# Kernel optimization log

Measured on AMD Instinct MI355X. Metric: run time of the kernel, lower is better.

## Reference

```python
import jax, jax.numpy as jnp
import numpy as np
import math

D_MODEL = 512
EXPAND = 2
D_INNER = EXPAND * D_MODEL          # 1024
HEADDIM = 8
NHEADS = D_INNER // HEADDIM         # 128
NGROUPS = 2
D_STATE = 16
CONV_DIM = D_INNER + 2 * NGROUPS * D_STATE   # 1088
D_IN_PROJ = 2 * D_INNER + 2 * NGROUPS * D_STATE + NHEADS  # 2240
P13 = [(0, 0), (1, 1)]
P31 = [(1, 1), (0, 0)]
P33 = [(1, 1), (1, 1)]


def silu(x):
    return x * jax.nn.sigmoid(x)


def dwconv(x, w, pad):
    # depthwise 2D conv; x: (B,C,H,W), w: (C,1,kh,kw)
    return jax.lax.conv_general_dilated(
        x, w, (1, 1), pad,
        dimension_numbers=('NCHW', 'OIHW', 'NCHW'),
        feature_group_count=x.shape[1])


def interleave_ch(a, b):
    # channel-interleave: out[:, ::2] = a, out[:, 1::2] = b
    Bn, C, Hh, Ww = a.shape
    return jnp.stack([a, b], axis=2).reshape(Bn, 2 * C, Hh, Ww)


def linear_attn(x, dt, A, Bm, Cm, Dp):
    # non-causal linear-attention duality of Mamba2 (grouped heads)
    # x: (B,L,h,p), dt: (B,L,h), A: (h,) negative, Bm/Cm: (B,L,g*ds), Dp: (h,)
    b, L, h, p = x.shape
    g, ds = NGROUPS, D_STATE
    dA = -(dt * A[None, None, :])          # ssd_positive_dA -> positive
    Vs = x * dA[..., None]
    K = Bm.reshape(b, L, g, ds)
    Q = Cm.reshape(b, L, g, ds)
    Vg = Vs.reshape(b, L, h // g, g, p)
    KV = jnp.einsum('blgs,blmgp->bmgsp', K, Vg)       # (b, h/g, g, ds, p)
    y = jnp.einsum('blgs,bmgsp->blmgp', Q, KV)        # (b, L, h/g, g, p)
    y = y + (x * Dp[None, None, :, None]).reshape(b, L, h // g, g, p)
    return y.reshape(b, L, h, p)


def setup_inputs() -> dict:
    key = jax.random.key(0)
    ks = jax.random.split(key, 20)
    Bn, Hh, Ww = 8, 64, 64
    L = Hh * Ww
    u = jax.random.normal(ks[0], (Bn, L, D_MODEL), jnp.float32)
    W_in = jax.random.normal(ks[1], (D_IN_PROJ, D_MODEL), jnp.float32) / math.sqrt(D_MODEL)
    dt = jnp.exp(jax.random.uniform(ks[2], (NHEADS,)) * (math.log(0.1) - math.log(0.001)) + math.log(0.001))
    dt = jnp.clip(dt, 1e-4, None)
    dt_bias = dt + jnp.log(-jnp.expm1(-dt))
    A_log = jnp.log(jax.random.uniform(ks[3], (NHEADS,), minval=1.0, maxval=16.0))
    Dp = jnp.ones((NHEADS,), jnp.float32)

    def cw(k, c, kh, kw):
        return jax.random.normal(k, (c, 1, kh, kw), jnp.float32) / math.sqrt(kh * kw)

    bcC = 2 * NGROUPS * D_STATE // 4  # 16
    w_conv2d = cw(ks[4], CONV_DIM // 2, 3, 3)
    w13x1 = cw(ks[5], D_INNER // 4, 1, 3)
    w31x1 = cw(ks[6], D_INNER // 4, 3, 1)
    w13x2 = cw(ks[7], D_INNER // 4, 1, 3)
    w31x2 = cw(ks[8], D_INNER // 4, 3, 1)
    w13bc1 = cw(ks[9], bcC, 1, 3)
    w31bc1 = cw(ks[10], bcC, 3, 1)
    w13bc2 = cw(ks[11], bcC, 1, 3)
    w31bc2 = cw(ks[12], bcC, 3, 1)
    w_conv2d_z = cw(ks[13], D_INNER, 3, 3)
    ln_g = jnp.ones((D_INNER,), jnp.float32)
    ln_b = jnp.zeros((D_INNER,), jnp.float32)
    scale = jnp.float32(1.0)
    shift = jnp.float32(0.0)
    alpha1 = jnp.float32(1.0)
    alpha2 = jnp.float32(1.0)
    W_out = jax.random.normal(ks[14], (D_MODEL, 2 * D_INNER), jnp.float32) / math.sqrt(2 * D_INNER)
    return dict(u=u, H=Hh, W=Ww, W_in=W_in, dt_bias=dt_bias, A_log=A_log, Dp=Dp,
                w_conv2d=w_conv2d, w13x1=w13x1, w31x1=w31x1, w13x2=w13x2, w31x2=w31x2,
                w13bc1=w13bc1, w31bc1=w31bc1, w13bc2=w13bc2, w31bc2=w31bc2,
                w_conv2d_z=w_conv2d_z, ln_g=ln_g, ln_b=ln_b, scale=scale, shift=shift,
                alpha1=alpha1, alpha2=alpha2, W_out=W_out)


def reference(u, H, W, W_in, dt_bias, A_log, Dp, w_conv2d, w13x1, w31x1, w13x2, w31x2,
              w13bc1, w31bc1, w13bc2, w31bc2, w_conv2d_z, ln_g, ln_b, scale, shift,
              alpha1, alpha2, W_out):
    Bn, L, _ = u.shape
    zxbcdt = u @ W_in.T                                 # (B,L,2240)
    z = zxbcdt[..., :D_INNER]
    xBC = zxbcdt[..., D_INNER:D_INNER + CONV_DIM]
    dt = zxbcdt[..., D_INNER + CONV_DIM:]
    dt = jax.nn.softplus(dt + dt_bias)                  # (B,L,h)

    # even/odd channel-interleave split, reshape to NCHW feature maps
    even = xBC[..., 0::2].reshape(Bn, H, W, -1).transpose(0, 3, 1, 2)
    odd = xBC[..., 1::2].reshape(Bn, H, W, -1).transpose(0, 3, 1, 2)
    even = silu(dwconv(even, w_conv2d, P33))

    oe = odd[:, 0::2]
    oo = odd[:, 1::2]
    x_oe, bc_oe = oe[:, :D_INNER // 4], oe[:, D_INNER // 4:]
    x_oo, bc_oo = oo[:, :D_INNER // 4], oo[:, D_INNER // 4:]
    x_oe = silu(dwconv(dwconv(x_oe, w31x1, P31), w13x1, P13))
    x_oo = silu(dwconv(dwconv(x_oo, w13x2, P13), w31x2, P31))
    bc_oe = silu(dwconv(dwconv(bc_oe, w13bc1, P13), w31bc1, P31))
    bc_oo = silu(dwconv(dwconv(bc_oo, w31bc2, P31), w13bc2, P13))
    xbc_oe = jnp.concatenate([x_oe, bc_oe], axis=1)
    xbc_oo = jnp.concatenate([x_oo, bc_oo], axis=1)
    odd = interleave_ch(xbc_oe, xbc_oo)

    xBCc = interleave_ch(even, odd)                     # (B, CONV_DIM, H, W)
    xBCc = xBCc.transpose(0, 2, 3, 1).reshape(Bn, L, CONV_DIM)
    x = xBCc[..., :D_INNER]
    Bm = xBCc[..., D_INNER:D_INNER + NGROUPS * D_STATE]
    Cm = xBCc[..., D_INNER + NGROUPS * D_STATE:]

    A = -jnp.exp(A_log)
    y = linear_attn(x.reshape(Bn, L, NHEADS, HEADDIM), dt, A, Bm, Cm, Dp)
    y = y.reshape(Bn, L, D_INNER)

    mu = y.mean(-1, keepdims=True)
    var = ((y - mu) ** 2).mean(-1, keepdims=True)
    y = (y - mu) / jnp.sqrt(var + 1e-5) * ln_g + ln_b
    y = y * scale + shift

    zc = z.reshape(Bn, H, W, D_INNER).transpose(0, 3, 1, 2)
    zc = silu(dwconv(zc, w_conv2d_z, P33))
    zc = zc.transpose(0, 2, 3, 1).reshape(Bn, L, D_INNER)

    out = jnp.concatenate([alpha1 * y, alpha2 * zc], axis=-1) @ W_out.T
    return out
```

## Files before the change

kernel.cpp:

```cpp
#include <hip/hip_runtime.h>
#include <hip/hip_bf16.h>
#include <cstdint>
#include <cstddef>

#define HDIM    64
#define WDIM    64
#define LPB     4096
#define DMODEL  512
#define DIN     1024
#define CONVD   1088
#define DPROJ   2240
#define NHEADS  128
#define NCV     2112

using f16    = _Float16;
using f16x4  = __attribute__((ext_vector_type(4))) _Float16;
using f16x8  = __attribute__((ext_vector_type(8))) _Float16;
using f32x4  = __attribute__((ext_vector_type(4))) float;

__device__ __forceinline__ float siluf(float x) { return x / (1.f + __expf(-x)); }

__device__ __forceinline__ void fma_mix_lo(float& acc, unsigned a, unsigned b) {
  asm("v_fma_mix_f32 %0, %1, %2, %0 op_sel_hi:[1,1,0]" : "+v"(acc) : "v"(a), "v"(b));
}
__device__ __forceinline__ void fma_mix_hi(float& acc, unsigned a, unsigned b) {
  asm("v_fma_mix_f32 %0, %1, %2, %0 op_sel:[1,1,0] op_sel_hi:[1,1,0]" : "+v"(acc) : "v"(a), "v"(b));
}
__device__ __forceinline__ void fmixl(float& acc, unsigned a, float b) {
  asm("v_fma_mix_f32 %0, %1, %2, %0 op_sel_hi:[1,0,0]" : "+v"(acc) : "v"(a), "v"(b));
}
__device__ __forceinline__ void fmixh(float& acc, unsigned a, float b) {
  asm("v_fma_mix_f32 %0, %1, %2, %0 op_sel:[1,0,0] op_sel_hi:[1,0,0]" : "+v"(acc) : "v"(a), "v"(b));
}

__global__ __launch_bounds__(256) void k_cvt(const float* __restrict__ in, f16* __restrict__ out) {
  size_t i = ((size_t)blockIdx.x * 256 + threadIdx.x) * 4;
  f32x4 v = *(const f32x4*)(in + i);
  f16x4 o;
  #pragma unroll
  for (int j = 0; j < 4; ++j) o[j] = (f16)v[j];
  *(f16x4*)(out + i) = o;
}

__global__ __launch_bounds__(256) void k_cvt_win(const float* __restrict__ W, f16* __restrict__ out) {
  int i = blockIdx.x * 256 + threadIdx.x;
  int row = i >> 9, col = i & 511;
  float v = (row < DPROJ) ? W[row * 512 + col] : 0.f;
  out[i] = (f16)v;
}

__global__ __launch_bounds__(256) void k_keff(const float* __restrict__ w33,
                       const float* __restrict__ w13x1, const float* __restrict__ w31x1,
                       const float* __restrict__ w13x2, const float* __restrict__ w31x2,
                       const float* __restrict__ w13bc1, const float* __restrict__ w31bc1,
                       const float* __restrict__ w13bc2, const float* __restrict__ w31bc2,
                       const float* __restrict__ wz,
                       f16* __restrict__ keffall) {
  int j = blockIdx.x * 256 + threadIdx.x;
  if (j >= NCV) return;
  if (j < 1024) {
    #pragma unroll
    for (int tap = 0; tap < 9; ++tap) keffall[tap * NCV + j] = (f16)wz[j * 9 + tap];
    return;
  }
  int jj = j - 1024;
  float kh[3] = {0,0,0}, kw[3] = {0,0,0};
  bool dense = ((jj & 1) == 0);
  if (!dense) {
    int m = jj >> 2;
    if ((jj & 3) == 1) {
      if (m < 256) { for (int t=0;t<3;++t){ kh[t]=w31x1[m*3+t];  kw[t]=w13x1[m*3+t];  } }
      else { int q=m-256; for (int t=0;t<3;++t){ kh[t]=w31bc1[q*3+t]; kw[t]=w13bc1[q*3+t]; } }
    } else {
      if (m < 256) { for (int t=0;t<3;++t){ kh[t]=w31x2[m*3+t];  kw[t]=w13x2[m*3+t];  } }
      else { int q=m-256; for (int t=0;t<3;++t){ kh[t]=w31bc2[q*3+t]; kw[t]=w13bc2[q*3+t]; } }
    }
  }
  #pragma unroll
  for (int dh = 0; dh < 3; ++dh)
    #pragma unroll
    for (int dw = 0; dw < 3; ++dw) {
      float v = dense ? w33[(jj >> 1) * 9 + dh*3 + dw] : kh[dh] * kw[dw];
      keffall[(dh*3 + dw) * NCV + j] = (f16)v;
    }
}

template<typename OutT>
__global__ __launch_bounds__(256) void k_gemmf(const f16* __restrict__ A, int lda,
                                               const f16* __restrict__ Bm, int ldb,
                                               OutT* __restrict__ C, int ldc,
                                               int Kseg, int NW, int ntn, int ntmn, long Cseg) {
  __shared__ __align__(16) f16 As[128 * 32];
  __shared__ __align__(16) f16 Bs[128 * 32];

  int nwg = gridDim.x, bid = blockIdx.x;
  int q = nwg >> 3, r = nwg & 7;
  int xcd = bid & 7, loc = bid >> 3;
  int wg  = (xcd < r ? xcd * (q + 1) : r * (q + 1) + (xcd - r) * q) + loc;
  int kseg = wg / ntmn;
  int rem  = wg - kseg * ntmn;
  long m0 = (long)(rem / ntn) * 128;
  long n0 = (long)(rem % ntn) * 128;
  const int kbase = kseg * Kseg;

  const int tid  = threadIdx.x;
  const int w    = tid >> 6, lane = tid & 63;
  const int wr   = w >> 1, wc = w & 1;

  f32x4 acc[4][4];
  #pragma unroll
  for (int i = 0; i < 4; ++i)
    #pragma unroll
    for (int j = 0; j < 4; ++j) acc[i][j] = (f32x4){0.f,0.f,0.f,0.f};

  const int srow = w * 16 + (lane >> 2);
  const int scol = (lane & 3) * 8;
  const long aoff = (m0 + srow) * (long)lda + scol + kbase;
  const long boff = (n0 + srow) * (long)ldb + scol + kbase;
  const int fr = lane & 15;
  const int kc = (lane >> 4) * 8;

  for (int k0 = 0; k0 < Kseg; k0 += 32) {
    #pragma unroll
    for (int i = 0; i < 2; ++i) {
      long ao = aoff + (long)i*64*lda + k0;
      long bo = boff + (long)i*64*ldb + k0;
      int ls = (i*4 + w) * 512;
      __builtin_amdgcn_global_load_lds((const __attribute__((address_space(1))) void*)(A + ao),
                                       (__attribute__((address_space(3))) void*)&As[ls], 16, 0, 0);
      __builtin_amdgcn_global_load_lds((const __attribute__((address_space(1))) void*)(Bm + bo),
                                       (__attribute__((address_space(3))) void*)&Bs[ls], 16, 0, 0);
    }
    __syncthreads();
    f16x8 af[4], bf[4];
    #pragma unroll
    for (int f = 0; f < 4; ++f) {
      af[f] = *(const f16x8*)&As[(wr*64 + f*16 + fr) * 32 + kc];
      bf[f] = *(const f16x8*)&Bs[(wc*64 + f*16 + fr) * 32 + kc];
    }
    #pragma unroll
    for (int i = 0; i < 4; ++i)
      #pragma unroll
      for (int j = 0; j < 4; ++j)
        acc[i][j] = __builtin_amdgcn_mfma_f32_16x16x32_f16(af[i], bf[j], acc[i][j], 0, 0, 0);
    __syncthreads();
  }

  OutT* Cb = C + (long)kseg * Cseg;
  const int cr = (lane >> 4) * 4;
  const int cc = lane & 15;
  #pragma unroll
  for (int i = 0; i < 4; ++i) {
    long rbase = m0 + wr*64 + i*16 + cr;
    #pragma unroll
    for (int j = 0; j < 4; ++j) {
      int col = (int)n0 + wc*64 + j*16 + cc;
      if (col < NW) {
        OutT* cp = Cb + rbase * (long)ldc + col;
        #pragma unroll
        for (int r = 0; r < 4; ++r) cp[(long)r * ldc] = (OutT)acc[i][j][r];
      }
    }
  }
}

__global__ __launch_bounds__(256) void k_red2(const float* __restrict__ part, long seg,
                                              float* __restrict__ out) {
  long i = ((long)blockIdx.x * 256 + threadIdx.x) * 4;
  f32x4 s0 = *(const f32x4*)(part + i);
  f32x4 s1 = *(const f32x4*)(part + seg + i);
  f32x4 o;
  #pragma unroll
  for (int j = 0; j < 4; ++j) o[j] = s0[j] + s1[j];
  *(f32x4*)(out + i) = o;
}

__global__ __launch_bounds__(320) void k_conv_all(const f16* __restrict__ zx,
                                                  const f16* __restrict__ keffall,
                                                  const float* __restrict__ a2_p,
                                                  const float* __restrict__ dt_bias,
                                                  const float* __restrict__ A_log,
                                                  f16* __restrict__ xbc,
                                                  f16* __restrict__ g2,
                                                  float* __restrict__ dAb) {
  int t = threadIdx.x;
  int bid = blockIdx.x, qq = gridDim.x >> 3;
  int l = (bid & 7) * qq + (bid >> 3);
  int h = (l >> 6) & 63, wq = l & 63;
  long rowbase = (long)l * DPROJ;

  if (t < 264) {
    int c = t * 8;
    float acc[8] = {0,0,0,0,0,0,0,0};
    #pragma unroll
    for (int dh = 0; dh < 3; ++dh) {
      int hh = h + dh - 1;
      if (hh < 0 || hh >= HDIM) continue;
      #pragma unroll
      for (int dw = 0; dw < 3; ++dw) {
        int ww = wq + dw - 1;
        if (ww < 0 || ww >= WDIM) continue;
        uint4 v  = *(const uint4*)&zx[rowbase + (long)((dh-1)*WDIM + (dw-1)) * DPROJ + c];
        uint4 wt = *(const uint4*)&keffall[(dh*3 + dw) * NCV + c];
        fma_mix_lo(acc[0], v.x, wt.x);  fma_mix_hi(acc[1], v.x, wt.x);
        fma_mix_lo(acc[2], v.y, wt.y);  fma_mix_hi(acc[3], v.y, wt.y);
        fma_mix_lo(acc[4], v.z, wt.z);  fma_mix_hi(acc[5], v.z, wt.z);
        fma_mix_lo(acc[6], v.w, wt.w);  fma_mix_hi(acc[7], v.w, wt.w);
      }
    }
    f16x8 o8;
    if (c < 1024) {
      float a2 = a2_p[0];
      #pragma unroll
      for (int j = 0; j < 8; ++j) o8[j] = (f16)(a2 * siluf(acc[j]));
      *(f16x8*)&g2[(long)l * 2048 + 1024 + c] = o8;
    } else {
      #pragma unroll
      for (int j = 0; j < 8; ++j) o8[j] = (f16)siluf(acc[j]);
      *(f16x8*)&xbc[(long)l * CONVD + (c - 1024)] = o8;
    }
  } else if (t < 280) {
    int hd = (t - 264) * 8;
    f16x8 x = *(const f16x8*)&zx[rowbase + NCV + hd];
    f32x4 o0, o1;
    #pragma unroll
    for (int j = 0; j < 8; ++j) {
      float xx = (float)x[j] + dt_bias[hd + j];
      float sp = (xx > 20.f) ? xx : log1pf(__expf(xx));
      float dv = sp * __expf(A_log[hd + j]);
      if (j < 4) o0[j] = dv; else o1[j-4] = dv;
    }
    *(f32x4*)&dAb[(long)l * 128 + hd]     = o0;
    *(f32x4*)&dAb[(long)l * 128 + hd + 4] = o1;
  }
}

__global__ __launch_bounds__(512) void k_kv_part(const f16* __restrict__ xbc,
                                                 const float* __restrict__ dA,
                                                 float* __restrict__ part) {
  int t = threadIdx.x;
  int m = t >> 3, p = t & 7;
  int lc = blockIdx.x, b = blockIdx.y;
  float acc0[16], acc1[16];
  #pragma unroll
  for (int s = 0; s < 16; ++s) { acc0[s] = 0.f; acc1[s] = 0.f; }
  long lbase = (long)b * LPB + lc * 32;
  #pragma unroll 2
  for (int li = 0; li < 32; ++li) {
    long row = lbase + li;
    const f16* xr = xbc + row * CONVD;
    float2 aa = *(const float2*)&dA[row * 128 + 2*m];
    float xv0 = (float)xr[16*m + p]     * aa.x;
    float xv1 = (float)xr[16*m + 8 + p] * aa.y;
    uint4 q0 = *(const uint4*)(xr + DIN);
    uint4 q1 = *(const uint4*)(xr + DIN + 8);
    uint4 q2 = *(const uint4*)(xr + DIN + 16);
    uint4 q3 = *(const uint4*)(xr + DIN + 24);
    unsigned a0[4] = {q0.x, q0.y, q0.z, q0.w};
    unsigned a1[4] = {q1.x, q1.y, q1.z, q1.w};
    unsigned a2v[4] = {q2.x, q2.y, q2.z, q2.w};
    unsigned a3[4] = {q3.x, q3.y, q3.z, q3.w};
    #pragma unroll
    for (int k = 0; k < 4; ++k) {
      fmixl(acc0[2*k],     a0[k], xv0);  fmixh(acc0[2*k+1],     a0[k], xv0);
      fmixl(acc0[8+2*k],   a1[k], xv0);  fmixh(acc0[8+2*k+1],   a1[k], xv0);
      fmixl(acc1[2*k],     a2v[k], xv1); fmixh(acc1[2*k+1],     a2v[k], xv1);
      fmixl(acc1[8+2*k],   a3[k], xv1);  fmixh(acc1[8+2*k+1],   a3[k], xv1);
    }
  }
  long base = ((long)(b*128 + lc)) * 16384 + (long)m * 256;
  #pragma unroll
  for (int s = 0; s < 16; ++s) {
    part[base + s*8 + p]       = acc0[s];
    part[base + 128 + s*8 + p] = acc1[s];
  }
}

__global__ __launch_bounds__(256) void k_kv_red(const float* __restrict__ part,
                                                float* __restrict__ KV) {
  int e = blockIdx.x * 256 + threadIdx.x;
  int b = blockIdx.y;
  float s = 0.f;
  #pragma unroll 4
  for (int lc = 0; lc < 128; ++lc) s += part[((long)(b*128 + lc)) * 16384 + e];
  KV[(long)b * 16384 + e] = s;
}

__global__ __launch_bounds__(256) void k_y_ln(const f16* __restrict__ xbc,
                                              const float* __restrict__ KV,
                                              const float* __restrict__ Dp,
                                              const float* __restrict__ ln_g,
                                              const float* __restrict__ ln_b,
                                              const float* __restrict__ sc_p,
                                              const float* __restrict__ sh_p,
                                              const float* __restrict__ a1_p,
                                              f16* __restrict__ g2) {
  __shared__ float Qs[32][32];
  __shared__ float red[2][8];
  int t = threadIdx.x;
  int hd = t >> 1, pb = (t & 1) * 4;
  int m = hd >> 1, g = hd & 1;
  int b = blockIdx.x >> 7;
  long l0 = (long)b * LPB + (blockIdx.x & 127) * 32;

  f32x4 kv[16];
  #pragma unroll
  for (int s = 0; s < 16; ++s)
    kv[s] = *(const f32x4*)&KV[(long)b * 16384 + m*256 + g*128 + s*8 + pb];

  if (t < 128) {
    int tok = t >> 2, q8 = (t & 3) * 8;
    f16x8 qv = *(const f16x8*)&xbc[(l0 + tok) * CONVD + 1056 + q8];
    #pragma unroll
    for (int j = 0; j < 8; ++j) Qs[tok][q8 + j] = (float)qv[j];
  }
  int c0 = hd*8 + pb;
  f32x4 lg = *(const f32x4*)&ln_g[c0];
  f32x4 lb = *(const f32x4*)&ln_b[c0];
  float dpv = Dp[hd];
  float sc = sc_p[0], sh = sh_p[0], a1 = a1_p[0];
  int wv = t >> 6, lane = t & 63;
  __syncthreads();

  for (int tok = 0; tok < 32; ++tok) {
    long row = l0 + tok;
    f16x4 xr4 = *(const f16x4*)&xbc[row * CONVD + c0];
    f32x4 yv;
    #pragma unroll
    for (int j = 0; j < 4; ++j) yv[j] = (float)xr4[j] * dpv;
    #pragma unroll
    for (int s = 0; s < 16; ++s) {
      float qv = Qs[tok][g*16 + s];
      #pragma unroll
      for (int j = 0; j < 4; ++j) yv[j] = fmaf(qv, kv[s][j], yv[j]);
    }
    float s1 = yv[0] + yv[1] + yv[2] + yv[3];
    float s2 = yv[0]*yv[0] + yv[1]*yv[1] + yv[2]*yv[2] + yv[3]*yv[3];
    #pragma unroll
    for (int off = 1; off < 64; off <<= 1) {
      s1 += __shfl_xor(s1, off, 64);
      s2 += __shfl_xor(s2, off, 64);
    }
    if (lane == 0) { red[tok & 1][wv*2] = s1; red[tok & 1][wv*2 + 1] = s2; }
    __syncthreads();
    const float* rr = red[tok & 1];
    float S1 = rr[0] + rr[2] + rr[4] + rr[6];
    float S2 = rr[1] + rr[3] + rr[5] + rr[7];
    float mu   = S1 * (1.f/1024.f);
    float var  = S2 * (1.f/1024.f) - mu*mu;
    float rstd = rsqrtf(var + 1e-5f);
    f16x4 o4;
    #pragma unroll
    for (int j = 0; j < 4; ++j) {
      float yn = (yv[j] - mu) * rstd * lg[j] + lb[j];
      o4[j] = (f16)(a1 * (yn * sc + sh));
    }
    *(f16x4*)&g2[row * 2048 + c0] = o4;
  }
}

extern "C" void kernel_launch(void* const* d_in, const int* in_sizes, int n_in,
                              void* d_out, int out_size, void* d_ws, size_t ws_size,
                              hipStream_t stream) {
  const float* u       = (const float*)d_in[0];
  const float* W_in    = (const float*)d_in[3];
  const float* dt_bias = (const float*)d_in[4];
  const float* A_log   = (const float*)d_in[5];
  const float* Dp      = (const float*)d_in[6];
  const float* w33     = (const float*)d_in[7];
  const float* w13x1   = (const float*)d_in[8];
  const float* w31x1   = (const float*)d_in[9];
  const float* w13x2   = (const float*)d_in[10];
  const float* w31x2   = (const float*)d_in[11];
  const float* w13bc1  = (const float*)d_in[12];
  const float* w31bc1  = (const float*)d_in[13];
  const float* w13bc2  = (const float*)d_in[14];
  const float* w31bc2  = (const float*)d_in[15];
  const float* wz      = (const float*)d_in[16];
  const float* ln_g    = (const float*)d_in[17];
  const float* ln_b    = (const float*)d_in[18];
  const float* sc      = (const float*)d_in[19];
  const float* sh      = (const float*)d_in[20];
  const float* a1      = (const float*)d_in[21];
  const float* a2      = (const float*)d_in[22];
  const float* W_out   = (const float*)d_in[23];

  const size_t B_G2   = 16777216;
  const size_t B_ZX   = 18350080;
  const size_t B_XBC  = 8912896;
  const size_t B_DA   = 2097152;
  const size_t B_KV   = 65536;
  const size_t perC   = B_G2 + B_ZX + B_XBC + B_DA + B_KV;
  const size_t persist = 2359296 + 2097152 + 38912;

  int C = 8;
  while (C > 1 && persist + (size_t)C * perC > ws_size) C >>= 1;
  const int nch = 8 / C;
  const int Mc  = C * LPB;

  char* p = (char*)d_ws;
  f16*   win_f   = (f16*)p;   p += 2359296;
  f16*   wout_f  = (f16*)p;   p += 2097152;
  f16*   keffall = (f16*)p;   p += 38912;
  char*  arena   = p;
  f16*   g2      = (f16*)arena;
  f16*   u_f     = (f16*)arena;
  p = arena + (size_t)C * B_G2;
  f16*   zx      = (f16*)p;   p += (size_t)C * B_ZX;
  f16*   xbc     = (f16*)p;   p += (size_t)C * B_XBC;
  float* dAb     = (float*)p; p += (size_t)C * B_DA;
  float* KV      = (float*)p; p += (size_t)C * B_KV;
  float* part  = (float*)zx;
  float* kpart = (float*)zx;

  k_cvt_win<<<4608, 256, 0, stream>>>(W_in, win_f);
  k_cvt    <<<1024, 256, 0, stream>>>(W_out, wout_f);
  k_keff   <<<9, 256, 0, stream>>>(w33, w13x1, w31x1, w13x2, w31x2,
                                   w13bc1, w31bc1, w13bc2, w31bc2, wz, keffall);

  for (int ch = 0; ch < nch; ++ch) {
    const float* uc   = u + (size_t)ch * Mc * 512;
    float*       outc = (float*)d_out + (size_t)ch * Mc * 512;
    const int ntm = Mc / 128;

    k_cvt<<<Mc/2, 256, 0, stream>>>(uc, u_f);

    k_gemmf<f16><<<ntm*18, 256, 0, stream>>>(u_f, 512, win_f, 512,
                                             zx, DPROJ, 512, DPROJ, 18, ntm*18, 0);

    k_conv_all<<<Mc, 320, 0, stream>>>(zx, keffall, a2, dt_bias, A_log,
                                       xbc, g2, dAb);

    k_kv_part <<<dim3(128, C), 512, 0, stream>>>(xbc, dAb, part);
    k_kv_red  <<<dim3(64, C), 256, 0, stream>>>(part, KV);
    k_y_ln    <<<C*128, 256, 0, stream>>>(xbc, KV, Dp, ln_g, ln_b, sc, sh, a1, g2);

    const long cseg = (long)Mc * 512;
    k_gemmf<float><<<ntm*4*2, 256, 0, stream>>>(g2, 2048, wout_f, 2048,
                                                kpart, 512, 1024, 512, 4, ntm*4, cseg);
    k_red2<<<Mc/2, 256, 0, stream>>>(kpart, cseg, outc);
  }
}
```

Before: 612.1 us.

## Store split-K partials as fp16 and give each conv thread two channel groups

The output GEMM's split-K partial sums are now written as fp16 instead of fp32, and the reduction kernel reads fp16 and adds in fp32. This halves the partial-buffer traffic at the cost of rounding each partial to fp16. The depthwise conv kernel shrinks from 320 to 192 threads per block, with each thread handling two 8-channel groups so more loads are in flight per thread. SiLU now uses a hardware reciprocal instead of a divide.

Measured after the change: 573.8 us. 1.07x faster.

```diff
diff --git a/kernel.cpp b/kernel.cpp
--- a/kernel.cpp
+++ b/kernel.cpp
@@ -19,6 +19,9 @@
 using f32x4  = __attribute__((ext_vector_type(4))) float;
 
 __device__ __forceinline__ float siluf(float x) { return x / (1.f + __expf(-x)); }
+__device__ __forceinline__ float fsilu(float x) {
+  return x * __builtin_amdgcn_rcpf(1.f + __expf(-x));
+}
 
 __device__ __forceinline__ void fma_mix_lo(float& acc, unsigned a, unsigned b) {
   asm("v_fma_mix_f32 %0, %1, %2, %0 op_sel_hi:[1,1,0]" : "+v"(acc) : "v"(a), "v"(b));
@@ -164,18 +167,18 @@
   }
 }
 
-__global__ __launch_bounds__(256) void k_red2(const float* __restrict__ part, long seg,
-                                              float* __restrict__ out) {
+__global__ __launch_bounds__(256) void k_red2h(const f16* __restrict__ part, long seg,
+                                               float* __restrict__ out) {
   long i = ((long)blockIdx.x * 256 + threadIdx.x) * 4;
-  f32x4 s0 = *(const f32x4*)(part + i);
-  f32x4 s1 = *(const f32x4*)(part + seg + i);
+  f16x4 s0 = *(const f16x4*)(part + i);
+  f16x4 s1 = *(const f16x4*)(part + seg + i);
   f32x4 o;
   #pragma unroll
-  for (int j = 0; j < 4; ++j) o[j] = s0[j] + s1[j];
+  for (int j = 0; j < 4; ++j) o[j] = (float)s0[j] + (float)s1[j];
   *(f32x4*)(out + i) = o;
 }
 
-__global__ __launch_bounds__(320) void k_conv_all(const f16* __restrict__ zx,
+__global__ __launch_bounds__(192) void k_conv_all(const f16* __restrict__ zx,
                                                   const f16* __restrict__ keffall,
                                                   const float* __restrict__ a2_p,
                                                   const float* __restrict__ dt_bias,
@@ -189,9 +192,11 @@
   int h = (l >> 6) & 63, wq = l & 63;
   long rowbase = (long)l * DPROJ;
 
-  if (t < 264) {
-    int c = t * 8;
-    float acc[8] = {0,0,0,0,0,0,0,0};
+  if (t < 132) {
+    int c0 = t * 8;
+    int c1 = 1056 + t * 8;
+    float acc0[8] = {0,0,0,0,0,0,0,0};
+    float acc1[8] = {0,0,0,0,0,0,0,0};
     #pragma unroll
     for (int dh = 0; dh < 3; ++dh) {
       int hh = h + dh - 1;
@@ -200,27 +205,42 @@
       for (int dw = 0; dw < 3; ++dw) {
         int ww = wq + dw - 1;
         if (ww < 0 || ww >= WDIM) continue;
-        uint4 v  = *(const uint4*)&zx[rowbase + (long)((dh-1)*WDIM + (dw-1)) * DPROJ + c];
-        uint4 wt = *(const uint4*)&keffall[(dh*3 + dw) * NCV + c];
-        fma_mix_lo(acc[0], v.x, wt.x);  fma_mix_hi(acc[1], v.x, wt.x);
-        fma_mix_lo(acc[2], v.y, wt.y);  fma_mix_hi(acc[3], v.y, wt.y);
-        fma_mix_lo(acc[4], v.z, wt.z);  fma_mix_hi(acc[5], v.z, wt.z);
-        fma_mix_lo(acc[6], v.w, wt.w);  fma_mix_hi(acc[7], v.w, wt.w);
+        long off = rowbase + (long)((dh-1)*WDIM + (dw-1)) * DPROJ;
+        uint4 va = *(const uint4*)&zx[off + c0];
+        uint4 vb = *(const uint4*)&zx[off + c1];
+        uint4 wa = *(const uint4*)&keffall[(dh*3 + dw) * NCV + c0];
+        uint4 wb = *(const uint4*)&keffall[(dh*3 + dw) * NCV + c1];
+        fma_mix_lo(acc0[0], va.x, wa.x);  fma_mix_hi(acc0[1], va.x, wa.x);
+        fma_mix_lo(acc1[0], vb.x, wb.x);  fma_mix_hi(acc1[1], vb.x, wb.x);
+        fma_mix_lo(acc0[2], va.y, wa.y);  fma_mix_hi(acc0[3], va.y, wa.y);
+        fma_mix_lo(acc1[2], vb.y, wb.y);  fma_mix_hi(acc1[3], vb.y, wb.y);
+        fma_mix_lo(acc0[4], va.z, wa.z);  fma_mix_hi(acc0[5], va.z, wa.z);
+        fma_mix_lo(acc1[4], vb.z, wb.z);  fma_mix_hi(acc1[5], vb.z, wb.z);
+        fma_mix_lo(acc0[6], va.w, wa.w);  fma_mix_hi(acc0[7], va.w, wa.w);
+        fma_mix_lo(acc1[6], vb.w, wb.w);  fma_mix_hi(acc1[7], vb.w, wb.w);
       }
     }
-    f16x8 o8;
-    if (c < 1024) {
-      float a2 = a2_p[0];
+    float a2 = a2_p[0];
+    {
+      f16x8 o8;
+      if (c0 < 1024) {
+        #pragma unroll
+        for (int j = 0; j < 8; ++j) o8[j] = (f16)(a2 * fsilu(acc0[j]));
+        *(f16x8*)&g2[(long)l * 2048 + 1024 + c0] = o8;
+      } else {
+        #pragma unroll
+        for (int j = 0; j < 8; ++j) o8[j] = (f16)fsilu(acc0[j]);
+        *(f16x8*)&xbc[(long)l * CONVD + (c0 - 1024)] = o8;
+      }
+    }
+    {
+      f16x8 o8;
       #pragma unroll
-      for (int j = 0; j < 8; ++j) o8[j] = (f16)(a2 * siluf(acc[j]));
-      *(f16x8*)&g2[(long)l * 2048 + 1024 + c] = o8;
-    } else {
-      #pragma unroll
-      for (int j = 0; j < 8; ++j) o8[j] = (f16)siluf(acc[j]);
-      *(f16x8*)&xbc[(long)l * CONVD + (c - 1024)] = o8;
-    }
-  } else if (t < 280) {
-    int hd = (t - 264) * 8;
+      for (int j = 0; j < 8; ++j) o8[j] = (f16)fsilu(acc1[j]);
+      *(f16x8*)&xbc[(long)l * CONVD + (c1 - 1024)] = o8;
+    }
+  } else if (t < 148) {
+    int hd = (t - 132) * 8;
     f16x8 x = *(const f16x8*)&zx[rowbase + NCV + hd];
     f32x4 o0, o1;
     #pragma unroll
@@ -410,8 +430,8 @@
   f16*   xbc     = (f16*)p;   p += (size_t)C * B_XBC;
   float* dAb     = (float*)p; p += (size_t)C * B_DA;
   float* KV      = (float*)p; p += (size_t)C * B_KV;
-  float* part  = (float*)zx;
-  float* kpart = (float*)zx;
+  float* part   = (float*)zx;
+  f16*   kpart  = (f16*)zx;
 
   k_cvt_win<<<4608, 256, 0, stream>>>(W_in, win_f);
   k_cvt    <<<1024, 256, 0, stream>>>(W_out, wout_f);
@@ -428,7 +448,7 @@
     k_gemmf<f16><<<ntm*18, 256, 0, stream>>>(u_f, 512, win_f, 512,
                                              zx, DPROJ, 512, DPROJ, 18, ntm*18, 0);
 
-    k_conv_all<<<Mc, 320, 0, stream>>>(zx, keffall, a2, dt_bias, A_log,
+    k_conv_all<<<Mc, 192, 0, stream>>>(zx, keffall, a2, dt_bias, A_log,
                                        xbc, g2, dAb);
 
     k_kv_part <<<dim3(128, C), 512, 0, stream>>>(xbc, dAb, part);
@@ -436,8 +456,8 @@
     k_y_ln    <<<C*128, 256, 0, stream>>>(xbc, KV, Dp, ln_g, ln_b, sc, sh, a1, g2);
 
     const long cseg = (long)Mc * 512;
-    k_gemmf<float><<<ntm*4*2, 256, 0, stream>>>(g2, 2048, wout_f, 2048,
-                                                kpart, 512, 1024, 512, 4, ntm*4, cseg);
-    k_red2<<<Mc/2, 256, 0, stream>>>(kpart, cseg, outc);
-  }
-}
+    k_gemmf<f16><<<ntm*4*2, 256, 0, stream>>>(g2, 2048, wout_f, 2048,
+                                              kpart, 512, 1024, 512, 4, ntm*4, cseg);
+    k_red2h<<<Mc/2, 256, 0, stream>>>(kpart, cseg, outc);
+  }
+}
```
